# Optimization experiments

Measured on AMD Instinct MI355X. Metric: run time of the kernel, lower is better.

Reference implementation:

```python
import jax, jax.numpy as jnp
import numpy as np

B, S, D, F = 32, 512, 1024, 4096
R_COMMON, R_DOMAIN, E = 16, 16, 8
ALPHA = 2.0


def setup_inputs() -> dict:
    key = jax.random.key(0)
    ks = jax.random.split(key, 12)
    sd = lambda k, shape: jax.random.normal(k, shape, dtype=jnp.float32) * (1.0 / np.sqrt(shape[-1]))
    return {
        "hidden_states": jax.random.normal(ks[0], (B, S, D), dtype=jnp.float32),
        "expert_ids": jax.random.randint(ks[1], (B,), 0, E, dtype=jnp.int32),
        # nn.Linear weights: [out_features, in_features]
        "wi": sd(ks[2], (F, D)),
        "wo": sd(ks[3], (D, F)),
        "common_wi_a": sd(ks[4], (R_COMMON, D)),
        "common_wi_b": sd(ks[5], (F, R_COMMON)),
        "common_wo_a": sd(ks[6], (R_COMMON, F)),
        "common_wo_b": sd(ks[7], (D, R_COMMON)),
        # stacked per-expert LoRA weights
        "experts_wi_a": sd(ks[8], (E, R_DOMAIN, D)),
        "experts_wi_b": sd(ks[9], (F, R_DOMAIN)) * jnp.ones((E, 1, 1)) * 0.0 + sd(ks[9], (E, F, R_DOMAIN)),
        "experts_wo_a": sd(ks[10], (E, R_DOMAIN, F)),
        "experts_wo_b": sd(ks[11], (E, D, R_DOMAIN)),
    }


def _expert_lora(x, expert_ids, Wa, Wb):
    """Per-row (dim 0) expert LoRA correction, vectorized via gather.

    x: [B, S, din]; Wa: [E, r, din]; Wb: [E, dout, r].
    Equivalent to the per-expert mask-gather/scatter-add loop since each
    row belongs to exactly one expert.
    """
    Ab = Wa[expert_ids]  # [B, r, din]
    Bb = Wb[expert_ids]  # [B, dout, r]
    low = jnp.einsum("bsd,brd->bsr", x, Ab)
    return ALPHA * jnp.einsum("bsr,bor->bso", low, Bb)


def reference(hidden_states, expert_ids, wi, wo,
              common_wi_a, common_wi_b, common_wo_a, common_wo_b,
              experts_wi_a, experts_wi_b, experts_wo_a, experts_wo_b):
    x = hidden_states
    hidden_i = jnp.einsum("bsd,fd->bsf", x, wi)
    hidden_i += ALPHA * jnp.einsum("bsr,fr->bsf", jnp.einsum("bsd,rd->bsr", x, common_wi_a), common_wi_b)
    hidden_i += _expert_lora(x, expert_ids, experts_wi_a, experts_wi_b)
    hidden_i = jax.nn.relu(hidden_i)  # dense_act_fn='relu'; dropout is identity (eval)
    hidden_o = jnp.einsum("bsf,df->bsd", hidden_i, wo)
    hidden_o += ALPHA * jnp.einsum("bsr,dr->bsd", jnp.einsum("bsf,rf->bsr", hidden_i, common_wo_a), common_wo_b)
    hidden_o += _expert_lora(hidden_i, expert_ids, experts_wo_a, experts_wo_b)
    return hidden_o
```

## Files before the change

### kernel.cpp

```cpp
#include <hip/hip_runtime.h>
#include <hip/hip_bf16.h>
#include <stdint.h>

#define B_ 32
#define S_ 512
#define D_ 1024
#define F_ 4096
#define N_ (B_*S_)
#define E_ 8
#define ALPHA_ 2.0f

#define LDA1 1088
#define LDA2 4160

typedef __hip_bfloat16 bf16;
typedef __attribute__((ext_vector_type(8))) short short8;
typedef __attribute__((ext_vector_type(8))) __bf16 bf16x8;
typedef __attribute__((ext_vector_type(4))) float f32x4;

__device__ __forceinline__ f32x4 mfma_bf16(short8 a, short8 b, f32x4 c) {
    return __builtin_amdgcn_mfma_f32_16x16x32_bf16(
        __builtin_bit_cast(bf16x8, a), __builtin_bit_cast(bf16x8, b), c, 0, 0, 0);
}

__device__ __forceinline__ void gload_lds16(const void* g, void* l) {
    __builtin_amdgcn_global_load_lds((const __attribute__((address_space(1))) void*)g,
                                     (__attribute__((address_space(3))) void*)l, 16, 0, 0);
}

__device__ __forceinline__ unsigned pack2(float a, float b) {
    unsigned short x = __builtin_bit_cast(unsigned short, __float2bfloat16(a));
    unsigned short y = __builtin_bit_cast(unsigned short, __float2bfloat16(b));
    return (unsigned)x | ((unsigned)y << 16);
}
__device__ __forceinline__ uint2 pack4(float4 v) {
    return make_uint2(pack2(v.x, v.y), pack2(v.z, v.w));
}

__global__ __launch_bounds__(256) void prep_w_kernel(
    const float* __restrict__ wi, const float* __restrict__ wo,
    const float* __restrict__ cwia, const float* __restrict__ cwib,
    const float* __restrict__ cwoa, const float* __restrict__ cwob,
    const float* __restrict__ ewia, const float* __restrict__ ewib,
    const float* __restrict__ ewoa, const float* __restrict__ ewob,
    bf16* __restrict__ wi_b, bf16* __restrict__ wo_b,
    bf16* __restrict__ ex1, bf16* __restrict__ ex2,
    bf16* __restrict__ wilo, bf16* __restrict__ wolo)
{
    const int tid0 = blockIdx.x * blockDim.x + threadIdx.x;
    const int stride = gridDim.x * blockDim.x;

    for (int i = tid0; i < F_*D_/4; i += stride) {
        ((uint2*)wi_b)[i] = pack4(((const float4*)wi)[i]);
        ((uint2*)wo_b)[i] = pack4(((const float4*)wo)[i]);
    }
    for (int i = tid0; i < E_*F_*16; i += stride) {
        int e = i >> 16; int rem = i & 0xFFFF; int f = rem >> 4; int r = rem & 15;
        bf16* dst = ex1 + (((size_t)e*F_ + f) << 6);
        dst[r]      = __float2bfloat16(cwib[f*16 + r]);
        dst[16 + r] = __float2bfloat16(ewib[(((size_t)e*F_ + f) << 4) + r]);
        dst[32 + r] = __float2bfloat16(0.f);
        dst[48 + r] = __float2bfloat16(0.f);
    }
    for (int i = tid0; i < E_*D_*16; i += stride) {
        int e = i >> 14; int rem = i & 0x3FFF; int d = rem >> 4; int r = rem & 15;
        bf16* dst = ex2 + (((size_t)e*D_ + d) << 6);
        dst[r]      = __float2bfloat16(cwob[d*16 + r]);
        dst[16 + r] = __float2bfloat16(ewob[(((size_t)e*D_ + d) << 4) + r]);
        dst[32 + r] = __float2bfloat16(0.f);
        dst[48 + r] = __float2bfloat16(0.f);
    }
    for (int i = tid0; i < E_*32*(D_/4); i += stride) {
        int e = i / (32*(D_/4)); int rem = i - e*(32*(D_/4));
        int r = rem / (D_/4); int c4 = (rem % (D_/4)) * 4;
        const float* src = (r < 16) ? (cwia + (size_t)r*D_ + c4)
                                    : (ewia + ((size_t)(e*16 + (r-16)))*D_ + c4);
        *(uint2*)(wilo + ((size_t)(e*32 + r))*D_ + c4) = pack4(*(const float4*)src);
    }
    for (int i = tid0; i < E_*32*(F_/4); i += stride) {
        int e = i / (32*(F_/4)); int rem = i - e*(32*(F_/4));
        int r = rem / (F_/4); int c4 = (rem % (F_/4)) * 4;
        const float* src = (r < 16) ? (cwoa + (size_t)r*F_ + c4)
                                    : (ewoa + ((size_t)(e*16 + (r-16)))*F_ + c4);
        *(uint2*)(wolo + ((size_t)(e*32 + r))*F_ + c4) = pack4(*(const float4*)src);
    }
}

__global__ __launch_bounds__(256) void prep_x_kernel(
    const float* __restrict__ x, bf16* __restrict__ A1)
{
    const int tid0 = blockIdx.x * blockDim.x + threadIdx.x;
    const int stride = gridDim.x * blockDim.x;
    for (int i = tid0; i < N_*(D_/4); i += stride) {
        int row = i >> 8; int c4 = (i & 255) << 2;
        float4 v = *(const float4*)(x + (size_t)i * 4);
        *(uint2*)(A1 + (size_t)row*LDA1 + c4) = pack4(v);
    }
    for (int i = tid0; i < N_*8; i += stride) {
        int row = i >> 3; int c = (i & 7) << 2;
        *(uint2*)(A1 + (size_t)row*LDA1 + 1056 + c) = make_uint2(0u, 0u);
    }
}

template<int K>
__global__ __launch_bounds__(256) void lowproj_kernel(
    const bf16* __restrict__ A, const bf16* __restrict__ W,
    const int* __restrict__ eids, bf16* __restrict__ Out,
    int lda, int kout)
{
    constexpr int BM = 64, BK = 64;
    __shared__ __align__(16) bf16 Asm[BM*BK];
    __shared__ __align__(16) bf16 Wsm[32*BK];

    const int tid = threadIdx.x;
    const int row0 = blockIdx.x * BM;
    const int e = eids[row0 >> 9];
    const int w = tid >> 6, lane = tid & 63;
    const int tr = tid >> 3, ts = tid & 7;
    const int lrow = lane & 15;
    const int lk16 = (lane >> 4) << 4;

    f32x4 acc[2] = {};

    int aoff, woff[2];
    { int r = w*16 + lrow; aoff = r*128 + (lk16 ^ ((r & 7) << 4)); }
    #pragma unroll
    for (int n = 0; n < 2; ++n) {
        int r = n*16 + lrow; woff[n] = r*128 + (lk16 ^ ((r & 7) << 4));
    }
    const bf16* Wp = W + (size_t)e * 32 * K;

    #pragma unroll 1
    for (int kt = 0; kt < K/BK; ++kt) {
        const int k0 = kt * BK;
        #pragma unroll
        for (int i = 0; i < 2; ++i) {
            int row = tr + 32*i;
            int slot = ts ^ (row & 7);
            gload_lds16(A + (size_t)(row0 + row)*lda + k0 + slot*8,
                        (char*)Asm + row*128 + ts*16);
        }
        {
            int row = tr;
            int slot = ts ^ (row & 7);
            gload_lds16(Wp + (size_t)row*K + k0 + slot*8,
                        (char*)Wsm + row*128 + ts*16);
        }
        __syncthreads();
        #pragma unroll
        for (int kk = 0; kk < 2; ++kk) {
            short8 a = *(const short8*)((const char*)Asm + (aoff ^ (kk << 6)));
            #pragma unroll
            for (int n = 0; n < 2; ++n) {
                short8 b = *(const short8*)((const char*)Wsm + (woff[n] ^ (kk << 6)));
                acc[n] = mfma_bf16(a, b, acc[n]);
            }
        }
        __syncthreads();
    }

    const int jrow = (lane >> 4) << 2;
    #pragma unroll
    for (int n = 0; n < 2; ++n) {
        #pragma unroll
        for (int j = 0; j < 4; ++j) {
            int r = row0 + w*16 + jrow + j;
            int c = n*16 + lrow;
            Out[(size_t)r*lda + kout + c] = __float2bfloat16(ALPHA_ * acc[n][j]);
        }
    }
    #pragma unroll
    for (int i = 0; i < 8; ++i) {
        int idx = tid*8 + i;
        int r = idx >> 5, c = idx & 31;
        Out[(size_t)(row0 + r)*lda + kout + 32 + c] = __float2bfloat16(0.f);
    }
}

#define DSREAD(base, off) (*(const short8*)((const char*)(base) + (off)))

#define STAGE4(gptr, ld, ldsbase)                                          \
    _Pragma("unroll")                                                      \
    for (int i_ = 0; i_ < 4; ++i_) {                                       \
        int row_ = tr + 64*i_;                                             \
        int slot_ = ts ^ (row_ & 7);                                       \
        gload_lds16((gptr) + (size_t)row_*(ld) + slot_*8,                  \
                    (char*)(ldsbase) + row_*128 + ts*16);                  \
    }

#define TILE_BODY(AC, BC, DOSTAGE, AN, BN, KTN)                            \
  {                                                                        \
    short8 af[4][2]; short8 bq[4][2];                                      \
                                     \
    _Pragma("unroll") for (int m = 0; m < 4; ++m)                          \
      _Pragma("unroll") for (int kk = 0; kk < 2; ++kk)                     \
        af[m][kk] = DSREAD(AC, aoff[m] ^ (kk << 6));                       \
    _Pragma("unroll") for (int n = 0; n < 2; ++n)                          \
      _Pragma("unroll") for (int kk = 0; kk < 2; ++kk)                     \
        bq[n][kk] = DSREAD(BC, boff[n] ^ (kk << 6));                       \
    __builtin_amdgcn_s_setprio(1);                                         \
    _Pragma("unroll") for (int m = 0; m < 4; ++m)                          \
      _Pragma("unroll") for (int n = 0; n < 2; ++n)                        \
        _Pragma("unroll") for (int kk = 0; kk < 2; ++kk)                   \
          acc[m][n] = mfma_bf16(af[m][kk], bq[n][kk], acc[m][n]);          \
    __builtin_amdgcn_s_setprio(0);                                         \
                                                   \
    _Pragma("unroll") for (int n = 2; n < 4; ++n)                          \
      _Pragma("unroll") for (int kk = 0; kk < 2; ++kk)                     \
        bq[n][kk] = DSREAD(BC, boff[n] ^ (kk << 6));                       \
    __builtin_amdgcn_s_setprio(1);                                         \
    _Pragma("unroll") for (int m = 0; m < 4; ++m)                          \
      _Pragma("unroll") for (int n = 2; n < 4; ++n)                        \
        _Pragma("unroll") for (int kk = 0; kk < 2; ++kk)                   \
          acc[m][n] = mfma_bf16(af[m][kk], bq[n][kk], acc[m][n]);          \
    __builtin_amdgcn_s_setprio(0);                                         \
           \
    _Pragma("unroll") for (int m = 0; m < 4; ++m)                          \
      _Pragma("unroll") for (int kk = 0; kk < 2; ++kk)                     \
        af[m][kk] = DSREAD(AC, aoff[m+4] ^ (kk << 6));                     \
    if (DOSTAGE) {                                                         \
        STAGE4(Ag + (size_t)(KTN)*64, LDAe, AN);                           \
        if ((KTN) < KMAIN_EL/64) { STAGE4(Bg + (size_t)(KTN)*64, LDBe, BN); } \
        else                     { STAGE4(Bxg, 64, BN); }                  \
    }                                                                      \
    __builtin_amdgcn_s_setprio(1);                                         \
    _Pragma("unroll") for (int m = 0; m < 4; ++m)                          \
      _Pragma("unroll") for (int n = 0; n < 2; ++n)                        \
        _Pragma("unroll") for (int kk = 0; kk < 2; ++kk)                   \
          acc[m+4][n] = mfma_bf16(af[m][kk], bq[n][kk], acc[m+4][n]);      \
    __builtin_amdgcn_s_setprio(0);                                         \
                                                             \
    __builtin_amdgcn_s_setprio(1);                                         \
    _Pragma("unroll") for (int m = 0; m < 4; ++m)                          \
      _Pragma("unroll") for (int n = 2; n < 4; ++n)                        \
        _Pragma("unroll") for (int kk = 0; kk < 2; ++kk)                   \
          acc[m+4][n] = mfma_bf16(af[m][kk], bq[n][kk], acc[m+4][n]);      \
    __builtin_amdgcn_s_setprio(0);                                         \
    __syncthreads();                                                       \
  }

template<int KMAIN_EL, int LDAe, int LDBe, int LDCe, int NCOLSe, bool RELU_BF16>
__global__ __launch_bounds__(512, 2) void gemm256_kernel(
    const bf16* __restrict__ A, const bf16* __restrict__ Bmain,
    const bf16* __restrict__ Bextra, const int* __restrict__ eids,
    void* __restrict__ C)
{
    constexpr int MT = N_/256;
    constexpr int NT = NCOLSe/256;
    constexpr int NWG = MT*NT;
    constexpr int KTILES = KMAIN_EL/64 + 1;
    static_assert((KTILES & 1) == 1, "pair loop + tail assumes odd KTILES");
    static_assert(NWG % 8 == 0, "xcd swizzle needs nwg%8==0");
    constexpr int CPX = NWG/8;

    __shared__ __align__(16) bf16 As[2][256*64];
    __shared__ __align__(16) bf16 Bs[2][256*64];

    const int bid = blockIdx.x;
    const int wg = (bid & 7) * CPX + (bid >> 3);
    const int mt = wg % MT, nt = wg / MT;
    const int arow0 = mt * 256, bcol0 = nt * 256;
    const int e = eids[arow0 >> 9];

    const int tid = threadIdx.x;
    const int lane = tid & 63;
    const int wid = tid >> 6;
    const int wm = wid >> 2, wn = wid & 3;
    const int tr = tid >> 3, ts = tid & 7;

    const bf16* Ag  = A + (size_t)arow0 * LDAe;
    const bf16* Bg  = Bmain + (size_t)bcol0 * LDBe;
    const bf16* Bxg = Bextra + ((size_t)e * NCOLSe + bcol0) * 64;

    int aoff[8], boff[4];
    const int lk16 = (lane >> 4) << 4;
    #pragma unroll
    for (int m = 0; m < 8; ++m) {
        int r = wm*128 + m*16 + (lane & 15);
        aoff[m] = r*128 + (lk16 ^ ((r & 7) << 4));
    }
    #pragma unroll
    for (int n = 0; n < 4; ++n) {
        int r = wn*64 + n*16 + (lane & 15);
        boff[n] = r*128 + (lk16 ^ ((r & 7) << 4));
    }

    f32x4 acc[8][4] = {};

    STAGE4(Ag, LDAe, As[0]);
    STAGE4(Bg, LDBe, Bs[0]);
    __syncthreads();

    #pragma unroll 1
    for (int kt = 0; kt < KTILES - 1; kt += 2) {
        TILE_BODY(As[0], Bs[0], true, As[1], Bs[1], kt + 1);
        TILE_BODY(As[1], Bs[1], true, As[0], Bs[0], kt + 2);
    }
    TILE_BODY(As[0], Bs[0], false, As[1], Bs[1], 0);

    const int jrow = (lane >> 4) << 2;
    if constexpr (RELU_BF16) {
        bf16* Cb = (bf16*)C;
        #pragma unroll
        for (int m = 0; m < 8; ++m)
            #pragma unroll
            for (int j = 0; j < 4; ++j) {
                size_t rbase = (size_t)(arow0 + wm*128 + m*16 + jrow + j) * LDCe;
                #pragma unroll
                for (int n = 0; n < 4; ++n) {
                    float v = acc[m][n][j];
                    v = v > 0.f ? v : 0.f;
                    Cb[rbase + bcol0 + wn*64 + n*16 + (lane & 15)] = __float2bfloat16(v);
                }
            }
    } else {
        float* Cf = (float*)C;
        #pragma unroll
        for (int m = 0; m < 8; ++m)
            #pragma unroll
            for (int j = 0; j < 4; ++j) {
                size_t rbase = (size_t)(arow0 + wm*128 + m*16 + jrow + j) * LDCe;
                #pragma unroll
                for (int n = 0; n < 4; ++n)
                    Cf[rbase + bcol0 + wn*64 + n*16 + (lane & 15)] = acc[m][n][j];
            }
    }
}

extern "C" void kernel_launch(void* const* d_in, const int* in_sizes, int n_in,
                              void* d_out, int out_size, void* d_ws, size_t ws_size,
                              hipStream_t stream)
{
    const float* x    = (const float*)d_in[0];
    const int*   eids = (const int*)d_in[1];
    const float* wi   = (const float*)d_in[2];
    const float* wo   = (const float*)d_in[3];
    const float* cwia = (const float*)d_in[4];
    const float* cwib = (const float*)d_in[5];
    const float* cwoa = (const float*)d_in[6];
    const float* cwob = (const float*)d_in[7];
    const float* ewia = (const float*)d_in[8];
    const float* ewib = (const float*)d_in[9];
    const float* ewoa = (const float*)d_in[10];
    const float* ewob = (const float*)d_in[11];

    char* p = (char*)d_ws;
    bf16* A1   = (bf16*)p; p += (size_t)N_*LDA1*sizeof(bf16);
    bf16* A2   = (bf16*)p; p += (size_t)N_*LDA2*sizeof(bf16);
    bf16* wi_b = (bf16*)p; p += (size_t)F_*D_*sizeof(bf16);
    bf16* wo_b = (bf16*)p; p += (size_t)D_*F_*sizeof(bf16);
    bf16* ex1  = (bf16*)p; p += (size_t)E_*F_*64*sizeof(bf16);
    bf16* ex2  = (bf16*)p; p += (size_t)E_*D_*64*sizeof(bf16);
    bf16* wilo = (bf16*)p; p += (size_t)E_*32*D_*sizeof(bf16);
    bf16* wolo = (bf16*)p; p += (size_t)E_*32*F_*sizeof(bf16);

    prep_w_kernel<<<dim3(512), dim3(256), 0, stream>>>(
        wi, wo, cwia, cwib, cwoa, cwob, ewia, ewib, ewoa, ewob,
        wi_b, wo_b, ex1, ex2, wilo, wolo);

    prep_x_kernel<<<dim3(2048), dim3(256), 0, stream>>>(x, A1);

    lowproj_kernel<D_><<<dim3(N_/64), dim3(256), 0, stream>>>(
        A1, wilo, eids, A1, LDA1, D_);

    gemm256_kernel<D_, LDA1, D_, LDA2, F_, true>
        <<<dim3((N_/256)*(F_/256)), dim3(512), 0, stream>>>(A1, wi_b, ex1, eids, A2);

    lowproj_kernel<F_><<<dim3(N_/64), dim3(256), 0, stream>>>(
        A2, wolo, eids, A2, LDA2, F_);

    gemm256_kernel<F_, LDA2, F_, D_, D_, false>
        <<<dim3((N_/256)*(D_/256)), dim3(512), 0, stream>>>(A2, wo_b, ex2, eids, d_out);

    (void)in_sizes; (void)n_in; (void)out_size; (void)ws_size;
}
```

Before: 474.5 us.

## Prefetch two K-tiles ahead with vmcnt waits and split barriers

The GEMM main loop now issues global-to-LDS loads two K-tiles ahead instead of one. It waits only for the older tile via `s_waitcnt vmcnt(8)` rather than draining everything with `__syncthreads`. Staging moves out of the middle of the compute body into the loop, after each buffer is consumed. Bare `s_barrier` calls are added between the MFMA sub-phases to keep waves in lockstep. This aims to hide more global-load latency, at the cost of extra barriers per tile and reliance on exact vmcnt counting.

```diff
diff --git a/kernel.cpp b/kernel.cpp
--- a/kernel.cpp
+++ b/kernel.cpp
@@ -178,6 +178,9 @@
 }
 
 #define DSREAD(base, off) (*(const short8*)((const char*)(base) + (off)))
+#define VMWAIT8 asm volatile("s_waitcnt vmcnt(8)" ::: "memory")
+#define VMWAIT0 asm volatile("s_waitcnt vmcnt(0)" ::: "memory")
+#define BAR __builtin_amdgcn_s_barrier()
 
 #define STAGE4(gptr, ld, ldsbase)                                          \
     _Pragma("unroll")                                                      \
@@ -188,10 +191,15 @@
                     (char*)(ldsbase) + row_*128 + ts*16);                  \
     }
 
-#define TILE_BODY(AC, BC, DOSTAGE, AN, BN, KTN)                            \
+#define STAGE_TILE(KTN, AL, BL)                                            \
+  { STAGE4(Ag + (size_t)(KTN)*64, LDAe, AL);                               \
+    if ((KTN) < KMAIN_EL/64) { STAGE4(Bg + (size_t)(KTN)*64, LDBe, BL); }  \
+    else                     { STAGE4(Bxg, 64, BL); } }
+
+#define TILE4(AC, BC)                                                      \
   {                                                                        \
     short8 af[4][2]; short8 bq[4][2];                                      \
-                                     \
+                                                             \
     _Pragma("unroll") for (int m = 0; m < 4; ++m)                          \
       _Pragma("unroll") for (int kk = 0; kk < 2; ++kk)                     \
         af[m][kk] = DSREAD(AC, aoff[m] ^ (kk << 6));                       \
@@ -204,7 +212,8 @@
         _Pragma("unroll") for (int kk = 0; kk < 2; ++kk)                   \
           acc[m][n] = mfma_bf16(af[m][kk], bq[n][kk], acc[m][n]);          \
     __builtin_amdgcn_s_setprio(0);                                         \
-                                                   \
+    BAR;                                                                   \
+                                                             \
     _Pragma("unroll") for (int n = 2; n < 4; ++n)                          \
       _Pragma("unroll") for (int kk = 0; kk < 2; ++kk)                     \
         bq[n][kk] = DSREAD(BC, boff[n] ^ (kk << 6));                       \
@@ -214,21 +223,18 @@
         _Pragma("unroll") for (int kk = 0; kk < 2; ++kk)                   \
           acc[m][n] = mfma_bf16(af[m][kk], bq[n][kk], acc[m][n]);          \
     __builtin_amdgcn_s_setprio(0);                                         \
-           \
+    BAR;                                                                   \
+                                                             \
     _Pragma("unroll") for (int m = 0; m < 4; ++m)                          \
       _Pragma("unroll") for (int kk = 0; kk < 2; ++kk)                     \
         af[m][kk] = DSREAD(AC, aoff[m+4] ^ (kk << 6));                     \
-    if (DOSTAGE) {                                                         \
-        STAGE4(Ag + (size_t)(KTN)*64, LDAe, AN);                           \
-        if ((KTN) < KMAIN_EL/64) { STAGE4(Bg + (size_t)(KTN)*64, LDBe, BN); } \
-        else                     { STAGE4(Bxg, 64, BN); }                  \
-    }                                                                      \
     __builtin_amdgcn_s_setprio(1);                                         \
     _Pragma("unroll") for (int m = 0; m < 4; ++m)                          \
       _Pragma("unroll") for (int n = 0; n < 2; ++n)                        \
         _Pragma("unroll") for (int kk = 0; kk < 2; ++kk)                   \
           acc[m+4][n] = mfma_bf16(af[m][kk], bq[n][kk], acc[m+4][n]);      \
     __builtin_amdgcn_s_setprio(0);                                         \
+    BAR;                                                                   \
                                                              \
     __builtin_amdgcn_s_setprio(1);                                         \
     _Pragma("unroll") for (int m = 0; m < 4; ++m)                          \
@@ -236,7 +242,7 @@
         _Pragma("unroll") for (int kk = 0; kk < 2; ++kk)                   \
           acc[m+4][n] = mfma_bf16(af[m][kk], bq[n][kk], acc[m+4][n]);      \
     __builtin_amdgcn_s_setprio(0);                                         \
-    __syncthreads();                                                       \
+    BAR;               \
   }
 
 template<int KMAIN_EL, int LDAe, int LDBe, int LDCe, int NCOLSe, bool RELU_BF16>
@@ -287,16 +293,21 @@
 
     f32x4 acc[8][4] = {};
 
-    STAGE4(Ag, LDAe, As[0]);
-    STAGE4(Bg, LDBe, Bs[0]);
-    __syncthreads();
+    STAGE_TILE(0, As[0], Bs[0]);
+    STAGE_TILE(1, As[1], Bs[1]);
+    VMWAIT8; BAR;
 
     #pragma unroll 1
-    for (int kt = 0; kt < KTILES - 1; kt += 2) {
-        TILE_BODY(As[0], Bs[0], true, As[1], Bs[1], kt + 1);
-        TILE_BODY(As[1], Bs[1], true, As[0], Bs[0], kt + 2);
-    }
-    TILE_BODY(As[0], Bs[0], false, As[1], Bs[1], 0);
+    for (int t = 0; t < KTILES - 1; t += 2) {
+        TILE4(As[0], Bs[0]);
+        STAGE_TILE(t + 2, As[0], Bs[0]);
+        VMWAIT8; BAR;
+        TILE4(As[1], Bs[1]);
+        if (t + 3 < KTILES) { STAGE_TILE(t + 3, As[1], Bs[1]); VMWAIT8; }
+        else                { VMWAIT0; }
+        BAR;
+    }
+    TILE4(As[0], Bs[0]);
 
     const int jrow = (lane >> 4) << 2;
     if constexpr (RELU_BF16) {
```

Result: slower. 493.3 us (+4.0%).
